# Optimization experiments

Measured on AMD Instinct MI355X. Metric: run time of the kernel, lower is better.

Reference implementation:

```python
import jax, jax.numpy as jnp
import numpy as np
import math

B, N, M, C, H = 8, 2048, 2048, 512, 8
DK = C // H
EPS_LN = 1e-5


def _layernorm(x, g, b):
    mu = jnp.mean(x, axis=-1, keepdims=True)
    var = jnp.var(x, axis=-1, keepdims=True)
    return (x - mu) / jnp.sqrt(var + EPS_LN) * g + b


def setup_inputs() -> dict:
    key = jax.random.key(0)
    ks = jax.random.split(key, 8)
    s = 0.02
    return {
        "cross_x": jax.random.normal(ks[0], (B, N, C), jnp.float32),
        "cross_y": jax.random.normal(ks[1], (B, M, C), jnp.float32),
        "ln_x_g": jnp.ones((C,), jnp.float32),
        "ln_x_b": jnp.zeros((C,), jnp.float32),
        "ln_y_g": jnp.ones((C,), jnp.float32),
        "ln_y_b": jnp.zeros((C,), jnp.float32),
        "Wq": jax.random.normal(ks[2], (C, C), jnp.float32) * s,
        "bq": jnp.zeros((C,), jnp.float32),
        "Wk": jax.random.normal(ks[3], (C, C), jnp.float32) * s,
        "bk": jnp.zeros((C,), jnp.float32),
        "Wv": jax.random.normal(ks[4], (C, C), jnp.float32) * s,
        "bv": jnp.zeros((C,), jnp.float32),
        "Wc": jax.random.normal(ks[5], (C, C), jnp.float32) * s,  # conv1x1 weight [out, in]
        "bc": jnp.zeros((C,), jnp.float32),
        "ln_o_g": jnp.ones((C,), jnp.float32),
        "ln_o_b": jnp.zeros((C,), jnp.float32),
    }


def reference(cross_x, cross_y, ln_x_g, ln_x_b, ln_y_g, ln_y_b,
              Wq, bq, Wk, bk, Wv, bv, Wc, bc, ln_o_g, ln_o_b):
    b, n, c = cross_x.shape
    m = cross_y.shape[1]
    xn = _layernorm(cross_x, ln_x_g, ln_x_b)
    yn = _layernorm(cross_y, ln_y_g, ln_y_b)
    # projections -> [B, H, seq, dk]
    q = (xn @ Wq + bq).reshape(b, n, H, DK).transpose(0, 2, 1, 3)
    k = (yn @ Wk + bk).reshape(b, m, H, DK).transpose(0, 2, 1, 3)
    v = (yn @ Wv + bv).reshape(b, m, H, DK).transpose(0, 2, 1, 3)
    scale = 1.0 / math.sqrt(DK)
    scores = jnp.einsum("bhnd,bhmd->bhnm", q, k) * scale
    attn = jax.nn.softmax(scores, axis=-1)
    # extra renormalization across the HEAD dimension (dim=1)
    attn = attn / (1e-9 + jnp.sum(attn, axis=1, keepdims=True))
    # dropout is identity in eval/reference mode
    o = jnp.einsum("bhnm,bhmd->bhnd", attn, v)
    q_flat = q.transpose(0, 2, 1, 3).reshape(b, n, c)  # [B, N, C]
    o_flat = o.transpose(0, 2, 1, 3).reshape(b, n, c)
    # conv1x1 over channels on (query - x)
    h = (q_flat - o_flat) @ Wc.T + bc
    h = jax.nn.leaky_relu(_layernorm(h, ln_o_g, ln_o_b), negative_slope=0.02)
    return q_flat + h
```

## Files before the change

kernel.cpp:

```cpp
#include <hip/hip_runtime.h>


typedef short bf16x8 __attribute__((ext_vector_type(8)));
typedef float f32x4 __attribute__((ext_vector_type(4)));

#define CS 0.18033688f

#define BARRIER_LG() do { __builtin_amdgcn_sched_barrier(0); \
  asm volatile("s_waitcnt lgkmcnt(0)" ::: "memory"); \
  __builtin_amdgcn_s_barrier(); \
  __builtin_amdgcn_sched_barrier(0); } while(0)

#define VMCNT(N) do { __builtin_amdgcn_sched_barrier(0); \
  asm volatile("s_waitcnt vmcnt(" #N ")" ::: "memory"); \
  __builtin_amdgcn_sched_barrier(0); } while(0)

__device__ inline float b2f(unsigned short u){
  union { unsigned int i; float f; } c; c.i = ((unsigned int)u) << 16; return c.f;
}
__device__ inline unsigned short f2b(float f){
  union { float ff; unsigned int i; } c; c.ff = f;
  unsigned int i = c.i;
  return (unsigned short)((i + 0x7FFFu + ((i >> 16) & 1u)) >> 16);
}
__device__ inline unsigned int cvtpk(float lo, float hi){
  unsigned int r;
  asm("v_cvt_pk_bf16_f32 %0, %1, %2" : "=v"(r) : "v"(lo), "v"(hi));
  return r;
}
__device__ inline float fast_rcp(float x){ return __builtin_amdgcn_rcpf(x); }
__device__ inline f32x4 mfma16(bf16x8 a, bf16x8 b, f32x4 c){
  return __builtin_amdgcn_mfma_f32_16x16x32_bf16(a, b, c, 0, 0, 0);
}
__device__ __forceinline__ void gl16(const unsigned short* g, unsigned short* l){
  __builtin_amdgcn_global_load_lds(
      (const __attribute__((address_space(1))) unsigned int*)g,
      (__attribute__((address_space(3))) unsigned int*)l,
      16, 0, 0);
}

__global__ void detect_dtype(const unsigned int* __restrict__ g, int* __restrict__ flag){
  *flag = (g[0] == 0x3F800000u) ? 1 : 0;
}

__global__ void zero_f32(float* __restrict__ p, int n){
  int i = blockIdx.x * 256 + threadIdx.x;
  if (i < n) p[i] = 0.0f;
}

__global__ void convert_misc(const void* Wc, const void* bq, const void* bk,
    const void* bv, const void* bc, const void* go, const void* bo,
    unsigned short* WcB, unsigned short* bqB, unsigned short* bkB,
    unsigned short* bvB, unsigned short* bcB, unsigned short* goB,
    unsigned short* boB, const int* __restrict__ flag){
  int i = blockIdx.x * 256 + threadIdx.x;
  const void* src; unsigned short* dst; int o;
  if (i < 262144){ src = Wc; dst = WcB; o = i; }
  else {
    int j = i - 262144; int seg = j >> 9; o = j & 511;
    if (seg == 0){ src = bq; dst = bqB; }
    else if (seg == 1){ src = bk; dst = bkB; }
    else if (seg == 2){ src = bv; dst = bvB; }
    else if (seg == 3){ src = bc; dst = bcB; }
    else if (seg == 4){ src = go; dst = goB; }
    else if (seg == 5){ src = bo; dst = boB; }
    else return;
  }
  if (*flag) dst[o] = f2b(((const float*)src)[o]);
  else       dst[o] = ((const unsigned short*)src)[o];
}

__global__ __launch_bounds__(128) void ln_rows(const void* __restrict__ xv,
    const void* __restrict__ gxv, const void* __restrict__ bxv,
    const void* __restrict__ yv, const void* __restrict__ gyv, const void* __restrict__ byv,
    unsigned short* __restrict__ outx, unsigned short* __restrict__ outy,
    const int* __restrict__ flag){
  int row = blockIdx.x & 16383;
  int sel = blockIdx.x >> 14;
  const void* src = sel ? yv : xv;
  const void* gv = sel ? gyv : gxv;
  const void* bv_ = sel ? byv : bxv;
  unsigned short* out = sel ? outy : outx;
  int t = threadIdx.x;
  float v0, v1, v2, v3, g0, g1, g2, g3, bb0, bb1, bb2, bb3;
  if (*flag){
    float4 xf = ((const float4*)((const float*)src + (size_t)row * 512))[t];
    v0 = xf.x; v1 = xf.y; v2 = xf.z; v3 = xf.w;
    float4 gf = ((const float4*)gv)[t];  g0 = gf.x; g1 = gf.y; g2 = gf.z; g3 = gf.w;
    float4 bf = ((const float4*)bv_)[t]; bb0 = bf.x; bb1 = bf.y; bb2 = bf.z; bb3 = bf.w;
  } else {
    ushort4 raw = ((const ushort4*)((const unsigned short*)src + (size_t)row * 512))[t];
    v0 = b2f(raw.x); v1 = b2f(raw.y); v2 = b2f(raw.z); v3 = b2f(raw.w);
    ushort4 gr = ((const ushort4*)gv)[t];  g0 = b2f(gr.x); g1 = b2f(gr.y); g2 = b2f(gr.z); g3 = b2f(gr.w);
    ushort4 br = ((const ushort4*)bv_)[t]; bb0 = b2f(br.x); bb1 = b2f(br.y); bb2 = b2f(br.z); bb3 = b2f(br.w);
  }
  float s = v0 + v1 + v2 + v3;
  float sq = v0*v0 + v1*v1 + v2*v2 + v3*v3;
  #pragma unroll
  for (int off = 32; off; off >>= 1){
    s += __shfl_down(s, off, 64);
    sq += __shfl_down(sq, off, 64);
  }
  __shared__ float red[4];
  if ((t & 63) == 0){ red[(t >> 6)*2] = s; red[(t >> 6)*2 + 1] = sq; }
  __syncthreads();
  s = red[0] + red[2]; sq = red[1] + red[3];
  float mu = s * (1.0f/512.0f);
  float rstd = rsqrtf(sq * (1.0f/512.0f) - mu*mu + 1e-5f);
  ushort4 o;
  o.x = f2b((v0 - mu)*rstd*g0 + bb0);
  o.y = f2b((v1 - mu)*rstd*g1 + bb1);
  o.z = f2b((v2 - mu)*rstd*g2 + bb2);
  o.w = f2b((v3 - mu)*rstd*g3 + bb3);
  ((ushort4*)(out + (size_t)row * 512))[t] = o;
}

__global__ __launch_bounds__(256) void transposeW(const void* __restrict__ wq,
    const void* __restrict__ wk, const void* __restrict__ wv,
    unsigned short* __restrict__ oq, unsigned short* __restrict__ ok,
    unsigned short* __restrict__ ov, const int* __restrict__ flag){
  __shared__ unsigned short tile[32][33];
  const void* in = (blockIdx.z == 0) ? wq : (blockIdx.z == 1) ? wk : wv;
  unsigned short* outp = (blockIdx.z == 0) ? oq : (blockIdx.z == 1) ? ok : ov;
  int k0 = blockIdx.x * 32, j0 = blockIdx.y * 32;
  int t = threadIdx.x;
  int r = t >> 3, c4 = (t & 7) * 4;
  if (*flag){
    float4 v = *(const float4*)((const float*)in + (size_t)(k0 + r) * 512 + j0 + c4);
    tile[r][c4] = f2b(v.x); tile[r][c4+1] = f2b(v.y);
    tile[r][c4+2] = f2b(v.z); tile[r][c4+3] = f2b(v.w);
  } else {
    ushort4 v = *(const ushort4*)((const unsigned short*)in + (size_t)(k0 + r) * 512 + j0 + c4);
    tile[r][c4] = v.x; tile[r][c4+1] = v.y; tile[r][c4+2] = v.z; tile[r][c4+3] = v.w;
  }
  __syncthreads();
  ushort4 o;
  o.x = tile[c4][r]; o.y = tile[c4+1][r]; o.z = tile[c4+2][r]; o.w = tile[c4+3][r];
  *(ushort4*)(outp + (size_t)(j0 + r) * 512 + k0 + c4) = o;
}

template<int OUT_MODE>
__global__ __launch_bounds__(256) void gemm_nt(const unsigned short* __restrict__ A,
    const unsigned short* __restrict__ Bt, const unsigned short* __restrict__ bias,
    void* __restrict__ Cout){
  __shared__ __align__(16) unsigned short As[128*32];
  __shared__ __align__(16) unsigned short Bs[128*32];
  int i0 = blockIdx.x * 128;
  int j0 = blockIdx.y * 128;
  int t = threadIdx.x;
  int w = t >> 6, lane = t & 63;
  int quad = lane >> 4, l15 = lane & 15;
  int wrow = (w >> 1) * 64, wcol = (w & 1) * 64;
  f32x4 acc[4][4];
  #pragma unroll
  for (int a = 0; a < 4; a++)
    #pragma unroll
    for (int b = 0; b < 4; b++)
      acc[a][b] = (f32x4){0.f, 0.f, 0.f, 0.f};

  int ra0 = t >> 2, ca0 = (t & 3) * 8;
  const unsigned short* Ag = A + (size_t)i0 * 512;
  const unsigned short* Bg = Bt + (size_t)j0 * 512;

  for (int kt = 0; kt < 16; kt++){
    int k0 = kt * 32;
    int4 av0 = *(const int4*)(Ag + (size_t)ra0 * 512 + k0 + ca0);
    int4 av1 = *(const int4*)(Ag + (size_t)(64 + ra0) * 512 + k0 + ca0);
    int4 bv0 = *(const int4*)(Bg + (size_t)ra0 * 512 + k0 + ca0);
    int4 bv1 = *(const int4*)(Bg + (size_t)(64 + ra0) * 512 + k0 + ca0);
    __syncthreads();
    ((int4*)As)[t] = av0; ((int4*)As)[t + 256] = av1;
    ((int4*)Bs)[t] = bv0; ((int4*)Bs)[t + 256] = bv1;
    __syncthreads();
    bf16x8 af[4], bfg[4];
    #pragma unroll
    for (int a = 0; a < 4; a++)
      af[a] = *(const bf16x8*)&As[(wrow + a*16 + l15)*32 + quad*8];
    #pragma unroll
    for (int b = 0; b < 4; b++)
      bfg[b] = *(const bf16x8*)&Bs[(wcol + b*16 + l15)*32 + quad*8];
    #pragma unroll
    for (int a = 0; a < 4; a++)
      #pragma unroll
      for (int b = 0; b < 4; b++)
        acc[a][b] = mfma16(af[a], bfg[b], acc[a][b]);
  }

  #pragma unroll
  for (int b = 0; b < 4; b++){
    int gcol = j0 + wcol + b*16 + l15;
    float bv = b2f(bias[gcol]);
    #pragma unroll
    for (int a = 0; a < 4; a++){
      #pragma unroll
      for (int r = 0; r < 4; r++){
        int grow = i0 + wrow + a*16 + quad*4 + r;
        float v = acc[a][b][r] + bv;
        if (OUT_MODE == 0){
          ((unsigned short*)Cout)[(size_t)grow*512 + gcol] = f2b(v);
        } else {
          int bb_ = grow >> 11, m = grow & 2047;
          int h = gcol >> 6, d = gcol & 63;
          ((unsigned short*)Cout)[(((size_t)(bb_*64 + (m >> 5))*512) + h*64 + d)*32
                                  + (m & 31)] = f2b(v);
        }
      }
    }
  }
}

__global__ __launch_bounds__(256) void attn_lsum(const unsigned short* __restrict__ Qm,
    const unsigned short* __restrict__ Km, float* __restrict__ Lsum){
  int wgl = blockIdx.x * 4 + (threadIdx.x >> 6);
  int b = wgl >> 9; int r_ = wgl & 511;
  int ntl = r_ >> 4; int ms = (r_ >> 2) & 3; int hg = r_ & 3;
  int h0 = hg * 2;
  int lane = threadIdx.x & 63, quad = lane >> 4, l15 = lane & 15;
  int n0 = ntl * 64;
  const unsigned short* Kp = Km + ((size_t)(b*2048)) * 512;
  bf16x8 aq[4][2][2];
  #pragma unroll
  for (int ns = 0; ns < 4; ns++)
    #pragma unroll
    for (int hh = 0; hh < 2; hh++)
      #pragma unroll
      for (int ks = 0; ks < 2; ks++)
        aq[ns][hh][ks] = *(const bf16x8*)(Qm + ((size_t)(b*2048 + n0 + ns*16 + l15))*512
                                          + (h0+hh)*64 + ks*32 + quad*8);
  float ls[4][2];
  #pragma unroll
  for (int ns = 0; ns < 4; ns++){ ls[ns][0] = 0.f; ls[ns][1] = 0.f; }
  for (int mt = 0; mt < 16; mt++){
    int m0 = ms*512 + mt*32;
    #pragma unroll
    for (int msub = 0; msub < 2; msub++){
      int mb = m0 + msub*16;
      #pragma unroll
      for (int hh = 0; hh < 2; hh++){
        bf16x8 ak0 = *(const bf16x8*)(Kp + (size_t)(mb + l15)*512 + (h0+hh)*64 + quad*8);
        bf16x8 ak1 = *(const bf16x8*)(Kp + (size_t)(mb + l15)*512 + (h0+hh)*64 + 32 + quad*8);
        #pragma unroll
        for (int ns = 0; ns < 4; ns++){
          f32x4 S = (f32x4){0.f,0.f,0.f,0.f};
          S = mfma16(ak0, aq[ns][hh][0], S);
          S = mfma16(ak1, aq[ns][hh][1], S);
          float e0 = exp2f(S[0]*CS), e1 = exp2f(S[1]*CS);
          float e2 = exp2f(S[2]*CS), e3 = exp2f(S[3]*CS);
          ls[ns][hh] += (e0 + e1) + (e2 + e3);
        }
      }
    }
  }
  #pragma unroll
  for (int ns = 0; ns < 4; ns++)
    #pragma unroll
    for (int hh = 0; hh < 2; hh++){
      float v = ls[ns][hh];
      v += __shfl_xor(v, 16, 64);
      v += __shfl_xor(v, 32, 64);
      ls[ns][hh] = v;
    }
  if (lane < 16){
    #pragma unroll
    for (int ns = 0; ns < 4; ns++)
      #pragma unroll
      for (int hh = 0; hh < 2; hh++)
        atomicAdd(&Lsum[(size_t)(b*8 + h0 + hh)*2048 + n0 + ns*16 + lane], ls[ns][hh]);
  }
}

__global__ __launch_bounds__(1024)
__attribute__((amdgpu_waves_per_eu(4, 4)))
void attn_out(const unsigned short* __restrict__ Qm,
    const unsigned short* __restrict__ Km, const unsigned short* __restrict__ VTm,
    const float* __restrict__ Lsum, unsigned short* __restrict__ DQO){
  __shared__ __align__(16) unsigned short Ks[32*512];
  __shared__ __align__(16) unsigned short Vs[512*32];
  __shared__ __align__(16) float ps[4*4*16*36];
  __shared__ __align__(16) unsigned short pbv[4*4*2*16*40];
  int bid = blockIdx.x;
  int b = bid & 7;
  int ntl = bid >> 3;
  int t = threadIdx.x;
  int w = t >> 6;
  int hp = w & 3;
  int nsub = w >> 2;
  int lane = t & 63, quad = lane >> 4, l15 = lane & 15;
  int h0 = hp * 2;
  int n0 = ntl * 64 + nsub * 16;
  int kx = (l15 & 7) << 4;

  const unsigned short* Kg = Km + (size_t)b * 1048576;
  const unsigned short* Vg = VTm + (size_t)b * 1048576;
  const unsigned short* Qp = Qm + ((size_t)(b*2048 + n0)) * 512;

  bf16x8 aq[2][2];
  #pragma unroll
  for (int hh = 0; hh < 2; hh++)
    #pragma unroll
    for (int ks = 0; ks < 2; ks++)
      aq[hh][ks] = *(const bf16x8*)(Qp + (size_t)l15*512 + (h0+hh)*64 + ks*32 + quad*8);
  float lg[2];
  #pragma unroll
  for (int hh = 0; hh < 2; hh++)
    lg[hh] = -log2f(Lsum[(size_t)(b*8 + h0 + hh)*2048 + n0 + l15]);
  f32x4 oacc[2][4];
  #pragma unroll
  for (int hh = 0; hh < 2; hh++)
    #pragma unroll
    for (int d = 0; d < 4; d++)
      oacc[hh][d] = (f32x4){0.f,0.f,0.f,0.f};

  int ksl = (lane ^ (w & 7)) << 3;
  unsigned short* kd0 = Ks + (w << 9);
  unsigned short* kd1 = Ks + ((w + 16) << 9);
  unsigned short* vd0 = Vs + t*8;
  unsigned short* vd1 = Vs + t*8 + 8192;

  float* psn = ps + nsub * 2304;
  float* pso = psn + hp * 576 + l15 * 36;
  unsigned short* pbn = pbv + nsub * 5120 + hp * 1280;

  gl16(Kg + ((size_t)(w     ) << 9) + ksl, kd0);
  gl16(Kg + ((size_t)(w + 16) << 9) + ksl, kd1);
  gl16(Vg + t*8, vd0);
  gl16(Vg + t*8 + 8192, vd1);

  for (int mt = 0; mt < 64; mt++){
    VMCNT(2);
    BARRIER_LG();
    float p[2][2][4];
    f32x4 s_own[2];
    #pragma unroll
    for (int msub = 0; msub < 2; msub++){
      const char* kr = (const char*)Ks + ((msub*16 + l15) << 10);
      #pragma unroll
      for (int hh = 0; hh < 2; hh++){
        int cb = (h0 + hh) * 128;
        bf16x8 k0 = *(const bf16x8*)(kr + ((cb + quad*16) ^ kx));
        bf16x8 k1 = *(const bf16x8*)(kr + ((cb + 64 + quad*16) ^ kx));
        f32x4 S = (f32x4){0.f,0.f,0.f,0.f};
        S = mfma16(k0, aq[hh][0], S);
        S = mfma16(k1, aq[hh][1], S);
        #pragma unroll
        for (int r = 0; r < 4; r++) p[hh][msub][r] = exp2f(fmaf(S[r], CS, lg[hh]));
      }
      f32x4 so;
      #pragma unroll
      for (int r = 0; r < 4; r++) so[r] = p[0][msub][r] + p[1][msub][r];
      s_own[msub] = so;
      *(f32x4*)(pso + msub*16 + quad*4) = so;
    }
    VMCNT(0);
    BARRIER_LG();
    if (mt < 63){
      const unsigned short* Kt = Kg + ((size_t)(mt+1) << 14);
      gl16(Kt + ((size_t)(w     ) << 9) + ksl, kd0);
      gl16(Kt + ((size_t)(w + 16) << 9) + ksl, kd1);
    }
    f32x4 ir4[2];
    #pragma unroll
    for (int msub = 0; msub < 2; msub++){
      f32x4 tt = s_own[msub];
      #pragma unroll
      for (int j = 1; j < 4; j++){
        int hq = (hp + j) & 3;
        tt += *(const f32x4*)(psn + hq*576 + l15*36 + msub*16 + quad*4);
      }
      f32x4 ir;
      #pragma unroll
      for (int r = 0; r < 4; r++) ir[r] = fast_rcp(1e-9f + tt[r]);
      ir4[msub] = ir;
    }
    #pragma unroll
    for (int hh = 0; hh < 2; hh++){
      #pragma unroll
      for (int msub = 0; msub < 2; msub++){
        int2 pv;
        pv.x = (int)cvtpk(p[hh][msub][0]*ir4[msub][0], p[hh][msub][1]*ir4[msub][1]);
        pv.y = (int)cvtpk(p[hh][msub][2]*ir4[msub][2], p[hh][msub][3]*ir4[msub][3]);
        *(int2*)&pbn[(hh*16 + l15)*40 + msub*16 + quad*4] = pv;
      }
    }
    #pragma unroll
    for (int hh = 0; hh < 2; hh++){
      bf16x8 wp = *(const bf16x8*)((const char*)pbn + (hh*16 + l15)*80 + quad*16);
      const char* vb = (const char*)Vs + (((h0+hh)*64 + l15) << 6) + quad*16;
      #pragma unroll
      for (int d = 0; d < 4; d++){
        bf16x8 vv = *(const bf16x8*)(vb + (d << 10));
        oacc[hh][d] = mfma16(vv, wp, oacc[hh][d]);
      }
    }
    BARRIER_LG();
    if (mt < 63){
      const unsigned short* Vt = Vg + ((size_t)(mt+1) << 14);
      gl16(Vt + t*8, vd0);
      gl16(Vt + t*8 + 8192, vd1);
    }
  }
  {
    size_t nrow = (size_t)(b*2048 + n0 + l15);
    const unsigned short* Qrow = Qm + nrow * 512;
    unsigned short* Drow = DQO + nrow * 512;
    #pragma unroll
    for (int hh = 0; hh < 2; hh++){
      #pragma unroll
      for (int d = 0; d < 4; d++){
        int c = (h0+hh)*64 + d*16 + quad*4;
        ushort4 qv = *(const ushort4*)(Qrow + c);
        ushort4 ov;
        ov.x = f2b(b2f(qv.x) - oacc[hh][d][0]);
        ov.y = f2b(b2f(qv.y) - oacc[hh][d][1]);
        ov.z = f2b(b2f(qv.z) - oacc[hh][d][2]);
        ov.w = f2b(b2f(qv.w) - oacc[hh][d][3]);
        *(ushort4*)(Drow + c) = ov;
      }
    }
  }
}

__global__ __launch_bounds__(128) void finalize_k(const unsigned short* __restrict__ H,
    const unsigned short* __restrict__ Qb, const unsigned short* __restrict__ g,
    const unsigned short* __restrict__ bb, void* __restrict__ outp,
    const int* __restrict__ flag){
  int row = blockIdx.x; int t = threadIdx.x;
  ushort4 hraw = ((const ushort4*)(H + (size_t)row * 512))[t];
  float h0 = b2f(hraw.x), h1 = b2f(hraw.y), h2 = b2f(hraw.z), h3 = b2f(hraw.w);
  float s = h0 + h1 + h2 + h3;
  float sq = h0*h0 + h1*h1 + h2*h2 + h3*h3;
  #pragma unroll
  for (int off = 32; off; off >>= 1){
    s += __shfl_down(s, off, 64);
    sq += __shfl_down(sq, off, 64);
  }
  __shared__ float red[4];
  if ((t & 63) == 0){ red[(t >> 6)*2] = s; red[(t >> 6)*2 + 1] = sq; }
  __syncthreads();
  s = red[0] + red[2]; sq = red[1] + red[3];
  float mu = s * (1.0f/512.0f);
  float rstd = rsqrtf(sq * (1.0f/512.0f) - mu*mu + 1e-5f);
  ushort4 gr = ((const ushort4*)g)[t];
  ushort4 br = ((const ushort4*)bb)[t];
  ushort4 qr = ((const ushort4*)(Qb + (size_t)row * 512))[t];
  float y0 = (h0 - mu)*rstd*b2f(gr.x) + b2f(br.x); y0 = fmaxf(y0, 0.02f*y0);
  float y1 = (h1 - mu)*rstd*b2f(gr.y) + b2f(br.y); y1 = fmaxf(y1, 0.02f*y1);
  float y2 = (h2 - mu)*rstd*b2f(gr.z) + b2f(br.z); y2 = fmaxf(y2, 0.02f*y2);
  float y3 = (h3 - mu)*rstd*b2f(gr.w) + b2f(br.w); y3 = fmaxf(y3, 0.02f*y3);
  float o0 = b2f(qr.x) + y0, o1 = b2f(qr.y) + y1, o2 = b2f(qr.z) + y2, o3 = b2f(qr.w) + y3;
  if (*flag){
    float4 o; o.x = o0; o.y = o1; o.z = o2; o.w = o3;
    ((float4*)((float*)outp + (size_t)row * 512))[t] = o;
  } else {
    ushort4 o; o.x = f2b(o0); o.y = f2b(o1); o.z = f2b(o2); o.w = f2b(o3);
    ((ushort4*)((unsigned short*)outp + (size_t)row * 512))[t] = o;
  }
}

extern "C" void kernel_launch(void* const* d_in, const int* in_sizes, int n_in,
                              void* d_out, int out_size, void* d_ws, size_t ws_size,
                              hipStream_t stream){
  const void* x      = d_in[0];
  const void* y      = d_in[1];
  const void* ln_x_g = d_in[2];
  const void* ln_x_b = d_in[3];
  const void* ln_y_g = d_in[4];
  const void* ln_y_b = d_in[5];
  const void* Wq     = d_in[6];
  const void* bq     = d_in[7];
  const void* Wk     = d_in[8];
  const void* bk     = d_in[9];
  const void* Wv     = d_in[10];
  const void* bv     = d_in[11];
  const void* Wc     = d_in[12];
  const void* bc     = d_in[13];
  const void* ln_o_g = d_in[14];
  const void* ln_o_b = d_in[15];

  const size_t MB = (size_t)1 << 20;
  char* ws = (char*)d_ws;
  unsigned short* Qb  = (unsigned short*)(ws);
  unsigned short* Kb  = (unsigned short*)(ws + 16*MB);
  unsigned short* VT  = (unsigned short*)(ws + 32*MB);
  unsigned short* XN  = (unsigned short*)(ws + 48*MB);
  unsigned short* YN  = (unsigned short*)(ws + 64*MB);
  unsigned short* DQO = XN;
  unsigned short* Hpre = YN;
  unsigned short* WqT = (unsigned short*)(ws + 80*MB);
  unsigned short* WkT = WqT + 512*512;
  unsigned short* WvT = WkT + 512*512;
  unsigned short* WcB = WvT + 512*512;
  unsigned short* bqB = (unsigned short*)(ws + 82*MB);
  unsigned short* bkB = bqB + 512;
  unsigned short* bvB = bkB + 512;
  unsigned short* bcB = bvB + 512;
  unsigned short* goB = bcB + 512;
  unsigned short* boB = goB + 512;
  float* Lsum         = (float*)(ws + 83*MB);
  int* Flag           = (int*)(ws + 84*MB);

  detect_dtype<<<dim3(1), dim3(1), 0, stream>>>((const unsigned int*)ln_x_g, Flag);
  zero_f32<<<dim3(512), dim3(256), 0, stream>>>(Lsum, 131072);
  convert_misc<<<dim3(1037), dim3(256), 0, stream>>>(Wc, bq, bk, bv, bc, ln_o_g, ln_o_b,
      WcB, bqB, bkB, bvB, bcB, goB, boB, Flag);
  ln_rows<<<dim3(32768), dim3(128), 0, stream>>>(x, ln_x_g, ln_x_b, y, ln_y_g, ln_y_b,
      XN, YN, Flag);
  transposeW<<<dim3(16,16,3), dim3(256), 0, stream>>>(Wq, Wk, Wv, WqT, WkT, WvT, Flag);
  gemm_nt<0><<<dim3(128,4), dim3(256), 0, stream>>>(XN, WqT, bqB, (void*)Qb);
  gemm_nt<0><<<dim3(128,4), dim3(256), 0, stream>>>(YN, WkT, bkB, (void*)Kb);
  gemm_nt<2><<<dim3(128,4), dim3(256), 0, stream>>>(YN, WvT, bvB, (void*)VT);
  attn_lsum<<<dim3(1024), dim3(256), 0, stream>>>(Qb, Kb, Lsum);
  attn_out<<<dim3(256), dim3(1024), 0, stream>>>(Qb, Kb, VT, Lsum, DQO);
  gemm_nt<0><<<dim3(128,4), dim3(256), 0, stream>>>(DQO, WcB, bcB, (void*)Hpre);
  finalize_k<<<dim3(16384), dim3(128), 0, stream>>>(Hpre, Qb, goB, boB, d_out, Flag);
}
```

Measured before the change: 525.0 us.

## Restructure attn_out into 512-thread blocks with 16-key tiles and double-buffered V

Each attention-output workgroup now has 512 threads and covers 32 query rows instead of 64, with twice as many blocks. Each iteration processes a 16-key tile instead of 32. The V tile is double-buffered and prefetched at the start of each iteration, and the P·V product uses 16x16x16 MFMAs fed directly from registers, so the LDS staging buffer for the bf16 probabilities is gone. The V-transpose layout in the GEMM epilogue changes to 16-element key groups to match. This trades less LDS use, higher occupancy and one fewer barrier per tile against twice as many loop iterations, more K/V reloads across blocks, and smaller MFMAs.

```diff
diff --git a/kernel.cpp b/kernel.cpp
--- a/kernel.cpp
+++ b/kernel.cpp
@@ -2,6 +2,7 @@
 
 
 typedef short bf16x8 __attribute__((ext_vector_type(8)));
+typedef short bf16x4 __attribute__((ext_vector_type(4)));
 typedef float f32x4 __attribute__((ext_vector_type(4)));
 
 #define CS 0.18033688f
@@ -31,6 +32,9 @@
 __device__ inline float fast_rcp(float x){ return __builtin_amdgcn_rcpf(x); }
 __device__ inline f32x4 mfma16(bf16x8 a, bf16x8 b, f32x4 c){
   return __builtin_amdgcn_mfma_f32_16x16x32_bf16(a, b, c, 0, 0, 0);
+}
+__device__ inline f32x4 mfma16k16(bf16x4 a, bf16x4 b, f32x4 c){
+  return __builtin_amdgcn_mfma_f32_16x16x16bf16_1k(a, b, c, 0, 0, 0);
 }
 __device__ __forceinline__ void gl16(const unsigned short* g, unsigned short* l){
   __builtin_amdgcn_global_load_lds(
@@ -201,8 +205,8 @@
         } else {
           int bb_ = grow >> 11, m = grow & 2047;
           int h = gcol >> 6, d = gcol & 63;
-          ((unsigned short*)Cout)[(((size_t)(bb_*64 + (m >> 5))*512) + h*64 + d)*32
-                                  + (m & 31)] = f2b(v);
+          ((unsigned short*)Cout)[(((size_t)(bb_*128 + (m >> 4))*512) + h*64 + d)*16
+                                  + (m & 15)] = f2b(v);
         }
       }
     }
@@ -269,15 +273,12 @@
   }
 }
 
-__global__ __launch_bounds__(1024)
-__attribute__((amdgpu_waves_per_eu(4, 4)))
-void attn_out(const unsigned short* __restrict__ Qm,
+__global__ __launch_bounds__(512) void attn_out(const unsigned short* __restrict__ Qm,
     const unsigned short* __restrict__ Km, const unsigned short* __restrict__ VTm,
     const float* __restrict__ Lsum, unsigned short* __restrict__ DQO){
-  __shared__ __align__(16) unsigned short Ks[32*512];
-  __shared__ __align__(16) unsigned short Vs[512*32];
-  __shared__ __align__(16) float ps[4*4*16*36];
-  __shared__ __align__(16) unsigned short pbv[4*4*2*16*40];
+  __shared__ __align__(16) unsigned short Ks[16*512];
+  __shared__ __align__(16) unsigned short Vsb[2][512*16];
+  __shared__ __align__(16) float ps[2*4*16*20];
   int bid = blockIdx.x;
   int b = bid & 7;
   int ntl = bid >> 3;
@@ -287,7 +288,7 @@
   int nsub = w >> 2;
   int lane = t & 63, quad = lane >> 4, l15 = lane & 15;
   int h0 = hp * 2;
-  int n0 = ntl * 64 + nsub * 16;
+  int n0 = ntl * 32 + nsub * 16;
   int kx = (l15 & 7) << 4;
 
   const unsigned short* Kg = Km + (size_t)b * 1048576;
@@ -311,29 +312,31 @@
     for (int d = 0; d < 4; d++)
       oacc[hh][d] = (f32x4){0.f,0.f,0.f,0.f};
 
-  int ksl = (lane ^ (w & 7)) << 3;
+  int ksl = (lane ^ w) << 3;
   unsigned short* kd0 = Ks + (w << 9);
-  unsigned short* kd1 = Ks + ((w + 16) << 9);
-  unsigned short* vd0 = Vs + t*8;
-  unsigned short* vd1 = Vs + t*8 + 8192;
-
-  float* psn = ps + nsub * 2304;
-  float* pso = psn + hp * 576 + l15 * 36;
-  unsigned short* pbn = pbv + nsub * 5120 + hp * 1280;
-
-  gl16(Kg + ((size_t)(w     ) << 9) + ksl, kd0);
-  gl16(Kg + ((size_t)(w + 16) << 9) + ksl, kd1);
-  gl16(Vg + t*8, vd0);
-  gl16(Vg + t*8 + 8192, vd1);
-
-  for (int mt = 0; mt < 64; mt++){
-    VMCNT(2);
+  unsigned short* kd1 = Ks + ((w + 8) << 9);
+
+  float* psn = ps + nsub * 1280;
+  float* pso = psn + hp * 320 + l15 * 20;
+
+  gl16(Kg + (w << 9) + ksl, kd0);
+  gl16(Kg + ((w + 8) << 9) + ksl, kd1);
+  gl16(Vg + t*8, Vsb[0] + t*8);
+  gl16(Vg + t*8 + 4096, Vsb[0] + t*8 + 4096);
+
+  for (int mt = 0; mt < 128; mt++){
+    VMCNT(0);
     BARRIER_LG();
-    float p[2][2][4];
-    f32x4 s_own[2];
-    #pragma unroll
-    for (int msub = 0; msub < 2; msub++){
-      const char* kr = (const char*)Ks + ((msub*16 + l15) << 10);
+    if (mt < 127){
+      unsigned short* vD = Vsb[(mt + 1) & 1];
+      const unsigned short* Vt = Vg + ((size_t)(mt + 1) << 13);
+      gl16(Vt + t*8, vD + t*8);
+      gl16(Vt + t*8 + 4096, vD + t*8 + 4096);
+    }
+    float p[2][4];
+    f32x4 so;
+    {
+      const char* kr = (const char*)Ks + (l15 << 10);
       #pragma unroll
       for (int hh = 0; hh < 2; hh++){
         int cb = (h0 + hh) * 128;
@@ -343,60 +346,38 @@
         S = mfma16(k0, aq[hh][0], S);
         S = mfma16(k1, aq[hh][1], S);
         #pragma unroll
-        for (int r = 0; r < 4; r++) p[hh][msub][r] = exp2f(fmaf(S[r], CS, lg[hh]));
+        for (int r = 0; r < 4; r++) p[hh][r] = exp2f(fmaf(S[r], CS, lg[hh]));
       }
-      f32x4 so;
-      #pragma unroll
-      for (int r = 0; r < 4; r++) so[r] = p[0][msub][r] + p[1][msub][r];
-      s_own[msub] = so;
-      *(f32x4*)(pso + msub*16 + quad*4) = so;
-    }
-    VMCNT(0);
+      #pragma unroll
+      for (int r = 0; r < 4; r++) so[r] = p[0][r] + p[1][r];
+      *(f32x4*)(pso + quad*4) = so;
+    }
     BARRIER_LG();
-    if (mt < 63){
-      const unsigned short* Kt = Kg + ((size_t)(mt+1) << 14);
-      gl16(Kt + ((size_t)(w     ) << 9) + ksl, kd0);
-      gl16(Kt + ((size_t)(w + 16) << 9) + ksl, kd1);
-    }
-    f32x4 ir4[2];
-    #pragma unroll
-    for (int msub = 0; msub < 2; msub++){
-      f32x4 tt = s_own[msub];
-      #pragma unroll
-      for (int j = 1; j < 4; j++){
-        int hq = (hp + j) & 3;
-        tt += *(const f32x4*)(psn + hq*576 + l15*36 + msub*16 + quad*4);
+    if (mt < 127){
+      const unsigned short* Kt = Kg + ((size_t)(mt + 1) << 13);
+      gl16(Kt + (w << 9) + ksl, kd0);
+      gl16(Kt + ((w + 8) << 9) + ksl, kd1);
+    }
+    f32x4 tt = so;
+    #pragma unroll
+    for (int j = 1; j < 4; j++){
+      int hq = (hp + j) & 3;
+      tt += *(const f32x4*)(psn + hq*320 + l15*20 + quad*4);
+    }
+    f32x4 ir;
+    #pragma unroll
+    for (int r = 0; r < 4; r++) ir[r] = fast_rcp(1e-9f + tt[r]);
+    const unsigned short* Vc = Vsb[mt & 1];
+    #pragma unroll
+    for (int hh = 0; hh < 2; hh++){
+      union { int2 i2; bf16x4 v; } pk;
+      pk.i2.x = (int)cvtpk(p[hh][0]*ir[0], p[hh][1]*ir[1]);
+      pk.i2.y = (int)cvtpk(p[hh][2]*ir[2], p[hh][3]*ir[3]);
+      #pragma unroll
+      for (int d = 0; d < 4; d++){
+        bf16x4 vv = *(const bf16x4*)(Vc + ((h0+hh)*64 + d*16 + l15)*16 + quad*4);
+        oacc[hh][d] = mfma16k16(vv, pk.v, oacc[hh][d]);
       }
-      f32x4 ir;
-      #pragma unroll
-      for (int r = 0; r < 4; r++) ir[r] = fast_rcp(1e-9f + tt[r]);
-      ir4[msub] = ir;
-    }
-    #pragma unroll
-    for (int hh = 0; hh < 2; hh++){
-      #pragma unroll
-      for (int msub = 0; msub < 2; msub++){
-        int2 pv;
-        pv.x = (int)cvtpk(p[hh][msub][0]*ir4[msub][0], p[hh][msub][1]*ir4[msub][1]);
-        pv.y = (int)cvtpk(p[hh][msub][2]*ir4[msub][2], p[hh][msub][3]*ir4[msub][3]);
-        *(int2*)&pbn[(hh*16 + l15)*40 + msub*16 + quad*4] = pv;
-      }
-    }
-    #pragma unroll
-    for (int hh = 0; hh < 2; hh++){
-      bf16x8 wp = *(const bf16x8*)((const char*)pbn + (hh*16 + l15)*80 + quad*16);
-      const char* vb = (const char*)Vs + (((h0+hh)*64 + l15) << 6) + quad*16;
-      #pragma unroll
-      for (int d = 0; d < 4; d++){
-        bf16x8 vv = *(const bf16x8*)(vb + (d << 10));
-        oacc[hh][d] = mfma16(vv, wp, oacc[hh][d]);
-      }
-    }
-    BARRIER_LG();
-    if (mt < 63){
-      const unsigned short* Vt = Vg + ((size_t)(mt+1) << 14);
-      gl16(Vt + t*8, vd0);
-      gl16(Vt + t*8 + 8192, vd1);
     }
   }
   {
@@ -510,7 +491,7 @@
   gemm_nt<0><<<dim3(128,4), dim3(256), 0, stream>>>(YN, WkT, bkB, (void*)Kb);
   gemm_nt<2><<<dim3(128,4), dim3(256), 0, stream>>>(YN, WvT, bvB, (void*)VT);
   attn_lsum<<<dim3(1024), dim3(256), 0, stream>>>(Qb, Kb, Lsum);
-  attn_out<<<dim3(256), dim3(1024), 0, stream>>>(Qb, Kb, VT, Lsum, DQO);
+  attn_out<<<dim3(512), dim3(512), 0, stream>>>(Qb, Kb, VT, Lsum, DQO);
   gemm_nt<0><<<dim3(128,4), dim3(256), 0, stream>>>(DQO, WcB, bcB, (void*)Hpre);
   finalize_k<<<dim3(16384), dim3(128), 0, stream>>>(Hpre, Qb, goB, boB, d_out, Flag);
 }
```

Result: slower. 559.9 us (+6.6%).
